# Optimization experiments

Measured on AMD Instinct MI355X. Metric: run time of the kernel, lower is better.

## Reference

```python
import jax, jax.numpy as jnp
import numpy as np

P, N, H, W, K = 100000, 8, 256, 256, 8
EPS = 1e-12  # F.normalize clamp_min eps


def setup_inputs() -> dict:
    key = jax.random.key(0)
    ks = jax.random.split(key, 12)
    normals = jax.random.normal(ks[3], (P, 3), jnp.float32)
    normals = normals / jnp.linalg.norm(normals, axis=-1, keepdims=True)
    return {
        "idx": jax.random.randint(ks[0], (N, H, W, K), 0, P),
        "dists": jax.random.uniform(ks[1], (N, H, W, K), dtype=jnp.float32),
        "points": jax.random.normal(ks[2], (P, 3), jnp.float32),
        "normals": normals,
        "light_location": jax.random.normal(ks[4], (1, 3), jnp.float32) * 2.0,
        "light_ambient": jax.random.uniform(ks[5], (1, 3), dtype=jnp.float32),
        "light_diffuse": jax.random.uniform(ks[6], (1, 3), dtype=jnp.float32),
        "light_specular": jax.random.uniform(ks[7], (1, 3), dtype=jnp.float32),
        "mat_ambient": jax.random.uniform(ks[8], (1, 3), dtype=jnp.float32),
        "mat_diffuse": jax.random.uniform(ks[9], (1, 3), dtype=jnp.float32),
        "mat_specular": jax.random.uniform(ks[10], (1, 3), dtype=jnp.float32),
        "camera_position": jax.random.normal(ks[11], (1, 3), jnp.float32) * 3.0,
        "shininess": 64,
    }


def _normalize(v):
    return v / jnp.clip(jnp.linalg.norm(v, axis=-1, keepdims=True), 1e-6)


def reference(idx, dists, points, normals, light_location, light_ambient,
              light_diffuse, light_specular, mat_ambient, mat_diffuse,
              mat_specular, camera_position, shininess):
    # masked gather: invalid (idx < 0) pixels read point 0
    safe_idx = jnp.where(idx < 0, 0, idx)                      # (N,H,W,K)
    pix_pts = points[safe_idx]                                 # (N,H,W,K,3)
    pix_nrm = normals[safe_idx]                                # (N,H,W,K,3)

    # point-light Phong shading (pytorch3d _apply_lighting)
    dir_light = _normalize(light_location - pix_pts)           # (N,H,W,K,3)
    cos = jnp.sum(pix_nrm * dir_light, axis=-1, keepdims=True)  # (N,H,W,K,1)
    diffuse = light_diffuse * jax.nn.relu(cos) * mat_diffuse

    view = _normalize(camera_position - pix_pts)
    reflect = 2.0 * cos * pix_nrm - dir_light
    alpha = jax.nn.relu(jnp.sum(view * reflect, axis=-1)) * (cos[..., 0] > 0)
    specular = light_specular * (alpha ** shininess)[..., None] * mat_specular

    ambient = light_ambient * mat_ambient                      # (1,3) broadcast
    colors = ambient + diffuse + specular                      # (N,H,W,K,3)

    # L1-normalized distance weights over K, weighted sum
    dist_mask = jnp.where(dists != -1.0, dists, 0.0)
    wn = dist_mask / jnp.clip(jnp.sum(jnp.abs(dist_mask), axis=-1, keepdims=True), EPS)
    images = jnp.sum(wn[..., None] * colors, axis=-2)          # (N,H,W,3)
    return images
```

## Files before the change

### kernel.cpp

```cpp
#include <hip/hip_runtime.h>

#define K 8

__global__ __launch_bounds__(256) void pack_pn_kernel(
    const float* __restrict__ points,
    const float* __restrict__ normals,
    float4*      __restrict__ rec,
    int P)
{
    const int i = blockIdx.x * blockDim.x + threadIdx.x;
    if (i >= P) return;
    const size_t b = (size_t)i * 3;
    rec[2 * i]     = make_float4(points[b],  points[b + 1],  points[b + 2],  0.0f);
    rec[2 * i + 1] = make_float4(normals[b], normals[b + 1], normals[b + 2], 0.0f);
}

struct ShadeConsts {
    float Lx, Ly, Lz, Cx, Cy, Cz;
    float amb0, amb1, amb2, dif0, dif1, dif2, spc0, spc1, spc2;
    int shin;
};

template <bool PACKED>
__global__ __launch_bounds__(256) void shading_compositor_kernel(
    const int*    __restrict__ idx,
    const float*  __restrict__ dists,
    const float*  __restrict__ points,
    const float*  __restrict__ normals,
    const float4* __restrict__ rec,
    const float*  __restrict__ light_location,
    const float*  __restrict__ light_ambient,
    const float*  __restrict__ light_diffuse,
    const float*  __restrict__ light_specular,
    const float*  __restrict__ mat_ambient,
    const float*  __restrict__ mat_diffuse,
    const float*  __restrict__ mat_specular,
    const float*  __restrict__ camera_position,
    const int*    __restrict__ shininess_p,
    float*        __restrict__ out,
    int n_pix)
{
    const int p = blockIdx.x * blockDim.x + threadIdx.x;
    if (p >= n_pix) return;

    const float Lx = light_location[0], Ly = light_location[1], Lz = light_location[2];
    const float Cx = camera_position[0], Cy = camera_position[1], Cz = camera_position[2];
    const float amb0 = light_ambient[0] * mat_ambient[0];
    const float amb1 = light_ambient[1] * mat_ambient[1];
    const float amb2 = light_ambient[2] * mat_ambient[2];
    const float dif0 = light_diffuse[0] * mat_diffuse[0];
    const float dif1 = light_diffuse[1] * mat_diffuse[1];
    const float dif2 = light_diffuse[2] * mat_diffuse[2];
    const float spc0 = light_specular[0] * mat_specular[0];
    const float spc1 = light_specular[1] * mat_specular[1];
    const float spc2 = light_specular[2] * mat_specular[2];
    const int   shin = shininess_p[0];

    const int4*   idxv = reinterpret_cast<const int4*>(idx   + (size_t)p * K);
    const float4* dstv = reinterpret_cast<const float4*>(dists + (size_t)p * K);
    int4   i0 = idxv[0], i1 = idxv[1];
    float4 d0 = dstv[0], d1 = dstv[1];

    int   ik[K] = {i0.x, i0.y, i0.z, i0.w, i1.x, i1.y, i1.z, i1.w};
    float dk[K] = {d0.x, d0.y, d0.z, d0.w, d1.x, d1.y, d1.z, d1.w};

    float w[K];
    float wsum = 0.f;
#pragma unroll
    for (int k = 0; k < K; ++k) {
        float d = dk[k];
        float m = (d != -1.0f) ? d : 0.0f;
        w[k] = m;
        wsum += fabsf(m);
    }
    const float winv = 1.0f / fmaxf(wsum, 1e-12f);

    float acc0 = 0.f, acc1 = 0.f, acc2 = 0.f;

#pragma unroll
    for (int k = 0; k < K; ++k) {
        const int ii = (ik[k] < 0) ? 0 : ik[k];
        float px, py, pz, nx, ny, nz;
        if (PACKED) {
            const float4 pr = rec[2 * (size_t)ii];
            const float4 nr = rec[2 * (size_t)ii + 1];
            px = pr.x; py = pr.y; pz = pr.z;
            nx = nr.x; ny = nr.y; nz = nr.z;
        } else {
            const size_t base = (size_t)ii * 3;
            px = points[base];  py = points[base + 1];  pz = points[base + 2];
            nx = normals[base]; ny = normals[base + 1]; nz = normals[base + 2];
        }

        float lx = Lx - px, ly = Ly - py, lz = Lz - pz;
        float ll = lx * lx + ly * ly + lz * lz;
        float li = (ll > 1e-12f) ? rsqrtf(ll) : 1e6f;
        lx *= li; ly *= li; lz *= li;

        const float cosv = nx * lx + ny * ly + nz * lz;

        float vx = Cx - px, vy = Cy - py, vz = Cz - pz;
        float vv = vx * vx + vy * vy + vz * vz;
        float vi = (vv > 1e-12f) ? rsqrtf(vv) : 1e6f;
        vx *= vi; vy *= vi; vz *= vi;

        const float c2 = 2.0f * cosv;
        const float rx = c2 * nx - lx;
        const float ry = c2 * ny - ly;
        const float rz = c2 * nz - lz;

        float alpha = fmaxf(vx * rx + vy * ry + vz * rz, 0.0f);
        if (!(cosv > 0.0f)) alpha = 0.0f;

        float sp = 1.0f, b = alpha;
        int e = shin;
        while (e > 0) {
            if (e & 1) sp *= b;
            b *= b;
            e >>= 1;
        }

        const float rc = fmaxf(cosv, 0.0f);
        const float wk = w[k];
        acc0 += wk * (amb0 + dif0 * rc + spc0 * sp);
        acc1 += wk * (amb1 + dif1 * rc + spc1 * sp);
        acc2 += wk * (amb2 + dif2 * rc + spc2 * sp);
    }

    float* o = out + (size_t)p * 3;
    o[0] = acc0 * winv;
    o[1] = acc1 * winv;
    o[2] = acc2 * winv;
}

extern "C" void kernel_launch(void* const* d_in, const int* in_sizes, int n_in,
                              void* d_out, int out_size, void* d_ws, size_t ws_size,
                              hipStream_t stream) {
    const int*   idx             = (const int*)d_in[0];
    const float* dists           = (const float*)d_in[1];
    const float* points          = (const float*)d_in[2];
    const float* normals         = (const float*)d_in[3];
    const float* light_location  = (const float*)d_in[4];
    const float* light_ambient   = (const float*)d_in[5];
    const float* light_diffuse   = (const float*)d_in[6];
    const float* light_specular  = (const float*)d_in[7];
    const float* mat_ambient     = (const float*)d_in[8];
    const float* mat_diffuse     = (const float*)d_in[9];
    const float* mat_specular    = (const float*)d_in[10];
    const float* camera_position = (const float*)d_in[11];
    const int*   shininess       = (const int*)d_in[12];
    float*       out             = (float*)d_out;

    const int n_pix = in_sizes[0] / K;
    const int P     = in_sizes[2] / 3;

    const int block = 256;
    const int grid  = (n_pix + block - 1) / block;

    const size_t need = (size_t)P * 2 * sizeof(float4);
    if (ws_size >= need) {
        float4* rec = (float4*)d_ws;
        pack_pn_kernel<<<(P + block - 1) / block, block, 0, stream>>>(points, normals, rec, P);
        shading_compositor_kernel<true><<<grid, block, 0, stream>>>(
            idx, dists, points, normals, rec, light_location, light_ambient,
            light_diffuse, light_specular, mat_ambient, mat_diffuse,
            mat_specular, camera_position, shininess, out, n_pix);
    } else {
        shading_compositor_kernel<false><<<grid, block, 0, stream>>>(
            idx, dists, points, normals, nullptr, light_location, light_ambient,
            light_diffuse, light_specular, mat_ambient, mat_diffuse,
            mat_specular, camera_position, shininess, out, n_pix);
    }
}
```

Baseline: 125.0 us.

## Precompute per-point Phong colors, then gather colors in a lightweight compositor

Shading depends only on the point, so a first kernel computes one RGB color per point into workspace, and a second kernel gathers those colors per pixel sample and applies the normalized distance weights. This replaces per-sample shading math and two 16-byte gathers with one 16-byte gather per sample. The per-pixel index/distance streams and outputs use nontemporal loads and stores. It adds a small extra pass over all points, even those never referenced.

```diff
diff --git a/kernel.cpp b/kernel.cpp
--- a/kernel.cpp
+++ b/kernel.cpp
@@ -2,32 +2,132 @@
 
 #define K 8
 
-__global__ __launch_bounds__(256) void pack_pn_kernel(
+typedef float f32x4 __attribute__((ext_vector_type(4)));
+typedef int   i32x4 __attribute__((ext_vector_type(4)));
+
+__global__ __launch_bounds__(256) void shade_points_kernel(
     const float* __restrict__ points,
     const float* __restrict__ normals,
-    float4*      __restrict__ rec,
+    const float* __restrict__ light_location,
+    const float* __restrict__ light_ambient,
+    const float* __restrict__ light_diffuse,
+    const float* __restrict__ light_specular,
+    const float* __restrict__ mat_ambient,
+    const float* __restrict__ mat_diffuse,
+    const float* __restrict__ mat_specular,
+    const float* __restrict__ camera_position,
+    const int*   __restrict__ shininess_p,
+    f32x4*       __restrict__ colors,
     int P)
 {
     const int i = blockIdx.x * blockDim.x + threadIdx.x;
     if (i >= P) return;
+
+    const float Lx = light_location[0], Ly = light_location[1], Lz = light_location[2];
+    const float Cx = camera_position[0], Cy = camera_position[1], Cz = camera_position[2];
+    const float amb0 = light_ambient[0] * mat_ambient[0];
+    const float amb1 = light_ambient[1] * mat_ambient[1];
+    const float amb2 = light_ambient[2] * mat_ambient[2];
+    const float dif0 = light_diffuse[0] * mat_diffuse[0];
+    const float dif1 = light_diffuse[1] * mat_diffuse[1];
+    const float dif2 = light_diffuse[2] * mat_diffuse[2];
+    const float spc0 = light_specular[0] * mat_specular[0];
+    const float spc1 = light_specular[1] * mat_specular[1];
+    const float spc2 = light_specular[2] * mat_specular[2];
+    const int   shin = shininess_p[0];
+
     const size_t b = (size_t)i * 3;
-    rec[2 * i]     = make_float4(points[b],  points[b + 1],  points[b + 2],  0.0f);
-    rec[2 * i + 1] = make_float4(normals[b], normals[b + 1], normals[b + 2], 0.0f);
-}
-
-struct ShadeConsts {
-    float Lx, Ly, Lz, Cx, Cy, Cz;
-    float amb0, amb1, amb2, dif0, dif1, dif2, spc0, spc1, spc2;
-    int shin;
-};
-
-template <bool PACKED>
-__global__ __launch_bounds__(256) void shading_compositor_kernel(
+    const float px = points[b],  py = points[b + 1],  pz = points[b + 2];
+    const float nx = normals[b], ny = normals[b + 1], nz = normals[b + 2];
+
+    float lx = Lx - px, ly = Ly - py, lz = Lz - pz;
+    float ll = lx * lx + ly * ly + lz * lz;
+    float li = (ll > 1e-12f) ? rsqrtf(ll) : 1e6f;
+    lx *= li; ly *= li; lz *= li;
+
+    const float cosv = nx * lx + ny * ly + nz * lz;
+
+    float vx = Cx - px, vy = Cy - py, vz = Cz - pz;
+    float vv = vx * vx + vy * vy + vz * vz;
+    float vi = (vv > 1e-12f) ? rsqrtf(vv) : 1e6f;
+    vx *= vi; vy *= vi; vz *= vi;
+
+    const float c2 = 2.0f * cosv;
+    const float rx = c2 * nx - lx;
+    const float ry = c2 * ny - ly;
+    const float rz = c2 * nz - lz;
+
+    float alpha = fmaxf(vx * rx + vy * ry + vz * rz, 0.0f);
+    if (!(cosv > 0.0f)) alpha = 0.0f;
+
+    float sp = 1.0f, bb = alpha;
+    int e = shin;
+    while (e > 0) {
+        if (e & 1) sp *= bb;
+        bb *= bb;
+        e >>= 1;
+    }
+
+    const float rc = fmaxf(cosv, 0.0f);
+    f32x4 c;
+    c.x = amb0 + dif0 * rc + spc0 * sp;
+    c.y = amb1 + dif1 * rc + spc1 * sp;
+    c.z = amb2 + dif2 * rc + spc2 * sp;
+    c.w = 0.0f;
+    colors[i] = c;
+}
+
+__global__ __launch_bounds__(256) void composite_kernel(
+    const int*   __restrict__ idx,
+    const float* __restrict__ dists,
+    const f32x4* __restrict__ colors,
+    float*       __restrict__ out,
+    int n_pix)
+{
+    const int p = blockIdx.x * blockDim.x + threadIdx.x;
+    if (p >= n_pix) return;
+
+    const i32x4* idxv = reinterpret_cast<const i32x4*>(idx + (size_t)p * K);
+    const f32x4* dstv = reinterpret_cast<const f32x4*>(dists + (size_t)p * K);
+    const i32x4 i0 = __builtin_nontemporal_load(idxv);
+    const i32x4 i1 = __builtin_nontemporal_load(idxv + 1);
+    const f32x4 d0 = __builtin_nontemporal_load(dstv);
+    const f32x4 d1 = __builtin_nontemporal_load(dstv + 1);
+
+    const int   ik[K] = {i0.x, i0.y, i0.z, i0.w, i1.x, i1.y, i1.z, i1.w};
+    const float dk[K] = {d0.x, d0.y, d0.z, d0.w, d1.x, d1.y, d1.z, d1.w};
+
+    f32x4 ck[K];
+#pragma unroll
+    for (int k = 0; k < K; ++k) {
+        const int ii = (ik[k] < 0) ? 0 : ik[k];
+        ck[k] = colors[ii];
+    }
+
+    float wsum = 0.f;
+    float acc0 = 0.f, acc1 = 0.f, acc2 = 0.f;
+#pragma unroll
+    for (int k = 0; k < K; ++k) {
+        const float d = dk[k];
+        const float m = (d != -1.0f) ? d : 0.0f;
+        wsum += fabsf(m);
+        acc0 += m * ck[k].x;
+        acc1 += m * ck[k].y;
+        acc2 += m * ck[k].z;
+    }
+    const float winv = 1.0f / fmaxf(wsum, 1e-12f);
+
+    float* o = out + (size_t)p * 3;
+    __builtin_nontemporal_store(acc0 * winv, o);
+    __builtin_nontemporal_store(acc1 * winv, o + 1);
+    __builtin_nontemporal_store(acc2 * winv, o + 2);
+}
+
+__global__ __launch_bounds__(256) void shading_compositor_fallback(
     const int*    __restrict__ idx,
     const float*  __restrict__ dists,
     const float*  __restrict__ points,
     const float*  __restrict__ normals,
-    const float4* __restrict__ rec,
     const float*  __restrict__ light_location,
     const float*  __restrict__ light_ambient,
     const float*  __restrict__ light_diffuse,
@@ -80,17 +180,9 @@
 #pragma unroll
     for (int k = 0; k < K; ++k) {
         const int ii = (ik[k] < 0) ? 0 : ik[k];
-        float px, py, pz, nx, ny, nz;
-        if (PACKED) {
-            const float4 pr = rec[2 * (size_t)ii];
-            const float4 nr = rec[2 * (size_t)ii + 1];
-            px = pr.x; py = pr.y; pz = pr.z;
-            nx = nr.x; ny = nr.y; nz = nr.z;
-        } else {
-            const size_t base = (size_t)ii * 3;
-            px = points[base];  py = points[base + 1];  pz = points[base + 2];
-            nx = normals[base]; ny = normals[base + 1]; nz = normals[base + 2];
-        }
+        const size_t base = (size_t)ii * 3;
+        const float px = points[base],  py = points[base + 1],  pz = points[base + 2];
+        const float nx = normals[base], ny = normals[base + 1], nz = normals[base + 2];
 
         float lx = Lx - px, ly = Ly - py, lz = Lz - pz;
         float ll = lx * lx + ly * ly + lz * lz;
@@ -112,11 +204,11 @@
         float alpha = fmaxf(vx * rx + vy * ry + vz * rz, 0.0f);
         if (!(cosv > 0.0f)) alpha = 0.0f;
 
-        float sp = 1.0f, b = alpha;
+        float sp = 1.0f, bb = alpha;
         int e = shin;
         while (e > 0) {
-            if (e & 1) sp *= b;
-            b *= b;
+            if (e & 1) sp *= bb;
+            bb *= bb;
             e >>= 1;
         }
 
@@ -157,18 +249,18 @@
     const int block = 256;
     const int grid  = (n_pix + block - 1) / block;
 
-    const size_t need = (size_t)P * 2 * sizeof(float4);
+    const size_t need = (size_t)P * sizeof(f32x4);
     if (ws_size >= need) {
-        float4* rec = (float4*)d_ws;
-        pack_pn_kernel<<<(P + block - 1) / block, block, 0, stream>>>(points, normals, rec, P);
-        shading_compositor_kernel<true><<<grid, block, 0, stream>>>(
-            idx, dists, points, normals, rec, light_location, light_ambient,
+        f32x4* colors = (f32x4*)d_ws;
+        shade_points_kernel<<<(P + block - 1) / block, block, 0, stream>>>(
+            points, normals, light_location, light_ambient, light_diffuse,
+            light_specular, mat_ambient, mat_diffuse, mat_specular,
+            camera_position, shininess, colors, P);
+        composite_kernel<<<grid, block, 0, stream>>>(idx, dists, colors, out, n_pix);
+    } else {
+        shading_compositor_fallback<<<grid, block, 0, stream>>>(
+            idx, dists, points, normals, light_location, light_ambient,
             light_diffuse, light_specular, mat_ambient, mat_diffuse,
             mat_specular, camera_position, shininess, out, n_pix);
-    } else {
-        shading_compositor_kernel<false><<<grid, block, 0, stream>>>(
-            idx, dists, points, normals, nullptr, light_location, light_ambient,
-            light_diffuse, light_specular, mat_ambient, mat_diffuse,
-            mat_specular, camera_position, shininess, out, n_pix);
-    }
-}
+    }
+}
```

Result: no change. 125.8 us (+0.6%).
